# Performance work log

Hardware: AMD Instinct MI355X
Metric: run time of the kernel (lower is better)

Reference implementation:

```python
import jax, jax.numpy as jnp
import numpy as np

BATCH, SEQ, DIM = 32, 1024, 512

def setup_inputs() -> dict:
    key = jax.random.key(0)
    k1, k2, k3 = jax.random.split(key, 3)
    scale = 1.0 / np.sqrt(DIM)
    return {
        "embedded_sequence": jax.random.normal(k1, (BATCH, SEQ, DIM), dtype=jnp.float32),
        "W_xh": jax.random.normal(k2, (DIM, DIM), dtype=jnp.float32) * scale,
        "W_hh": jax.random.normal(k3, (DIM, DIM), dtype=jnp.float32) * scale,
        "b": jnp.zeros((DIM,), dtype=jnp.float32),
    }

def reference(embedded_sequence, W_xh, W_hh, b):
    # SimpleRNN: h_t = tanh(x_t @ W_xh + h_{t-1} @ W_hh + b)
    B, T, D = embedded_sequence.shape
    # Precompute input projection for all timesteps (one big GEMM)
    xw = jnp.einsum('btd,de->bte', embedded_sequence, W_xh) + b  # [B,T,D]
    h0 = jnp.zeros((B, D), dtype=embedded_sequence.dtype)

    def step(h, xw_t):
        h_new = jnp.tanh(xw_t + h @ W_hh)
        return h_new, h_new

    h_final, seq_out = jax.lax.scan(step, h0, jnp.swapaxes(xw, 0, 1))  # scan over T
    seq_out = jnp.swapaxes(seq_out, 0, 1)  # [B,T,D]
    return (seq_out, h_final)
```

## Files before the change

### kernel.cpp

```cpp
#include <hip/hip_runtime.h>
#include <hip/hip_fp16.h>

#define BATCH 32
#define SEQ   1024
#define DIM   512

typedef _Float16 f16x8 __attribute__((ext_vector_type(8)));
typedef float    f32x4 __attribute__((ext_vector_type(4)));
typedef unsigned int u32x4 __attribute__((ext_vector_type(4)));

union UU4 { uint4 s; u32x4 v; };

static __device__ __forceinline__ float tanh_fast(float x) {
    float e = __expf(2.0f * x);
    return 1.0f - 2.0f / (e + 1.0f);
}

__global__ void pack_w2(const float* __restrict__ W0, __half* __restrict__ Wp0,
                        const float* __restrict__ W1, __half* __restrict__ Wp1) {
    int blk = blockIdx.x;
    const float* W  = (blk < 512) ? W0 : W1;
    __half*      Wp = (blk < 512) ? Wp0 : Wp1;
    int id = (blk & 511) * blockDim.x + threadIdx.x;
    int n = id & 511;
    int k = id >> 9;
    Wp[((k >> 5) * 512 + n) * 32 + ((k >> 3) & 3) * 8 + (k & 7)] = __float2half(W[k * 512 + n]);
}

__global__ __launch_bounds__(1024, 1) void gemm_xw(const float* __restrict__ X,
                                                   const __half* __restrict__ Wp,
                                                   const float* __restrict__ bias,
                                                   float* __restrict__ out) {
    const int nb   = blockIdx.x;
    const int mb   = blockIdx.y;
    const int lane = threadIdx.x & 63;
    const int wave = threadIdx.x >> 6;
    const int q    = lane >> 4;
    const int r16  = lane & 15;
    const int row  = mb * 256 + wave * 16 + r16;

    const float4* Xf4  = (const float4*)X;
    const uint4*  WpU4 = (const uint4*)Wp;

    f32x4 acc[16];
    #pragma unroll
    for (int nt = 0; nt < 16; ++nt) acc[nt] = (f32x4){0.f, 0.f, 0.f, 0.f};

    #pragma unroll 2
    for (int kb = 0; kb < 16; ++kb) {
        float4 a0 = Xf4[row * 128 + kb * 8 + q * 2];
        float4 a1 = Xf4[row * 128 + kb * 8 + q * 2 + 1];
        f16x8 af;
        af[0] = (_Float16)a0.x; af[1] = (_Float16)a0.y;
        af[2] = (_Float16)a0.z; af[3] = (_Float16)a0.w;
        af[4] = (_Float16)a1.x; af[5] = (_Float16)a1.y;
        af[6] = (_Float16)a1.z; af[7] = (_Float16)a1.w;
        #pragma unroll
        for (int nt = 0; nt < 16; ++nt) {
            int col = nb * 256 + nt * 16 + r16;
            UU4 tmp; tmp.s = WpU4[(kb * 512 + col) * 4 + q];
            acc[nt] = __builtin_amdgcn_mfma_f32_16x16x32_f16(
                af, __builtin_bit_cast(f16x8, tmp.v), acc[nt], 0, 0, 0);
        }
    }

    const int rbase = mb * 256 + wave * 16 + q * 4;
    #pragma unroll
    for (int nt = 0; nt < 16; ++nt) {
        int col = nb * 256 + nt * 16 + r16;
        float bv = bias[col];
        #pragma unroll
        for (int rr = 0; rr < 4; ++rr) {
            out[(size_t)(rbase + rr) * 512 + col] = acc[nt][rr] + bv;
        }
    }
}

__global__ __launch_bounds__(512, 2) void rnn_rec(const uint4* __restrict__ Wp4,
                                                  float* __restrict__ out) {
    extern __shared__ char smem[];
    uint4*  LBS = (uint4*)smem;
    __half* hb  = (__half*)(smem + 131072);

    const int b    = blockIdx.x;
    const int t    = threadIdx.x;
    const int lane = t & 63;
    const int w    = t >> 6;
    const int q    = lane >> 4;
    const int r16  = lane & 15;

    #pragma unroll
    for (int j = 0; j < 16; ++j) {
        int kb  = 12 + (j >> 2);
        int col = w * 64 + (j & 3) * 16 + r16;
        LBS[j * 512 + t] = Wp4[(kb * 512 + col) * 4 + q];
    }

    u32x4 Bf[48];
    #pragma unroll
    for (int kb = 0; kb < 12; ++kb) {
        #pragma unroll
        for (int nt = 0; nt < 4; ++nt) {
            int col = w * 64 + nt * 16 + r16;
            UU4 tmp; tmp.s = Wp4[(kb * 512 + col) * 4 + q];
            Bf[kb * 4 + nt] = tmp.v;
        }
    }
    #pragma unroll
    for (int i = 0; i < 48; ++i) asm volatile("" : "+a"(Bf[i]));

    float* orow = out + (size_t)b * SEQ * DIM;
    const int c = w * 64 + q * 16 + r16;

    float xw = orow[c];
    float h  = tanh_fast(xw);
    orow[c] = h;
    hb[c] = __float2half(h);
    xw = orow[DIM + c];
    __syncthreads();

    #pragma unroll 1
    for (int step = 1; step < SEQ; ++step) {
        orow += DIM;
        const __half* ha = hb + (((step & 1) ^ 1) << 9);

        f32x4 m[4];
        #pragma unroll
        for (int i = 0; i < 4; ++i) m[i] = (f32x4){0.f, 0.f, 0.f, 0.f};

        #pragma unroll
        for (int s = 0; s < 4; ++s) {
            f16x8 af = *(const f16x8*)(ha + (12 + s) * 32 + q * 8);
            #pragma unroll
            for (int nt = 0; nt < 4; ++nt) {
                UU4 tmp; tmp.s = LBS[(s * 4 + nt) * 512 + t];
                m[nt] = __builtin_amdgcn_mfma_f32_16x16x32_f16(
                    af, __builtin_bit_cast(f16x8, tmp.v), m[nt], 0, 0, 0);
            }
        }
        #pragma unroll
        for (int kb = 0; kb < 12; ++kb) {
            f16x8 af = *(const f16x8*)(ha + kb * 32 + q * 8);
            #pragma unroll
            for (int nt = 0; nt < 4; ++nt) {
                m[nt] = __builtin_amdgcn_mfma_f32_16x16x32_f16(
                    af, __builtin_bit_cast(f16x8, Bf[kb * 4 + nt]), m[nt], 0, 0, 0);
            }
        }

        float v = (q == 0 ? m[0][0] : q == 1 ? m[1][0] : q == 2 ? m[2][0] : m[3][0]) + xw;
        h = tanh_fast(v);

        orow[c] = h;
        __half* hw = hb + ((step & 1) << 9);
        hw[c] = __float2half(h);
        xw = orow[DIM + c];
        __syncthreads();
    }

    float* hf = out + (size_t)BATCH * SEQ * DIM + (size_t)b * DIM;
    hf[c] = h;
}

extern "C" void kernel_launch(void* const* d_in, const int* in_sizes, int n_in,
                              void* d_out, int out_size, void* d_ws, size_t ws_size,
                              hipStream_t stream) {
    const float* X    = (const float*)d_in[0];
    const float* Wxh  = (const float*)d_in[1];
    const float* Whh  = (const float*)d_in[2];
    const float* bias = (const float*)d_in[3];
    float* out = (float*)d_out;

    __half* WpXh = (__half*)d_ws;
    __half* WpHh = (__half*)((char*)d_ws + (512u << 10));

    (void)hipFuncSetAttribute((const void*)rnn_rec,
                              hipFuncAttributeMaxDynamicSharedMemorySize, 133120);

    pack_w2<<<1024, 512, 0, stream>>>(Wxh, WpXh, Whh, WpHh);
    gemm_xw<<<dim3(2, 128), 1024, 0, stream>>>(X, WpXh, bias, out);
    rnn_rec<<<BATCH, 512, 133120, stream>>>((const uint4*)WpHh, out);
}
```

Baseline: 1.480 ms.

## Fuse input GEMM into recurrence kernel with per-chunk flag gating

Merges the input-projection GEMM and the recurrent scan into one launch. The first 32 blocks run the recurrence while the other 512 blocks compute 128-timestep chunks of xW+b and publish completion through atomic flags. Recurrence blocks spin-wait on a chunk's flag only when they reach it, so the GEMM overlaps the serial scan instead of running before it. This relies on the recurrence blocks being co-resident with the GEMM blocks and adds spin-waits and atomics. It also needs 133KB of shared memory for every block, including the GEMM blocks, which may limit how many GEMM blocks can be resident at once.

```diff
diff --git a/kernel.cpp b/kernel.cpp
--- a/kernel.cpp
+++ b/kernel.cpp
@@ -16,8 +16,19 @@
     return 1.0f - 2.0f / (e + 1.0f);
 }
 
+static __device__ __forceinline__ void gate_wait(unsigned int* flags, int idx) {
+    if (threadIdx.x == 0) {
+        while (__hip_atomic_load(&flags[idx], __ATOMIC_ACQUIRE,
+                                 __HIP_MEMORY_SCOPE_AGENT) < 2u)
+            __builtin_amdgcn_s_sleep(8);
+    }
+    __syncthreads();
+}
+
 __global__ void pack_w2(const float* __restrict__ W0, __half* __restrict__ Wp0,
-                        const float* __restrict__ W1, __half* __restrict__ Wp1) {
+                        const float* __restrict__ W1, __half* __restrict__ Wp1,
+                        unsigned int* __restrict__ flags) {
+    if (blockIdx.x == 0 && threadIdx.x < 256) flags[threadIdx.x] = 0u;
     int blk = blockIdx.x;
     const float* W  = (blk < 512) ? W0 : W1;
     __half*      Wp = (blk < 512) ? Wp0 : Wp1;
@@ -27,73 +38,81 @@
     Wp[((k >> 5) * 512 + n) * 32 + ((k >> 3) & 3) * 8 + (k & 7)] = __float2half(W[k * 512 + n]);
 }
 
-__global__ __launch_bounds__(1024, 1) void gemm_xw(const float* __restrict__ X,
-                                                   const __half* __restrict__ Wp,
-                                                   const float* __restrict__ bias,
-                                                   float* __restrict__ out) {
-    const int nb   = blockIdx.x;
-    const int mb   = blockIdx.y;
+__global__ __launch_bounds__(512, 2) void fused_rnn(
+        const float* __restrict__ X, const __half* __restrict__ WpXh,
+        const float* __restrict__ bias, const uint4* __restrict__ WpHh4,
+        float* __restrict__ out, unsigned int* __restrict__ flags)
+{
+    extern __shared__ char smem[];
     const int lane = threadIdx.x & 63;
-    const int wave = threadIdx.x >> 6;
+    const int w    = threadIdx.x >> 6;
     const int q    = lane >> 4;
     const int r16  = lane & 15;
-    const int row  = mb * 256 + wave * 16 + r16;
-
-    const float4* Xf4  = (const float4*)X;
-    const uint4*  WpU4 = (const uint4*)Wp;
-
-    f32x4 acc[16];
-    #pragma unroll
-    for (int nt = 0; nt < 16; ++nt) acc[nt] = (f32x4){0.f, 0.f, 0.f, 0.f};
-
-    #pragma unroll 2
-    for (int kb = 0; kb < 16; ++kb) {
-        float4 a0 = Xf4[row * 128 + kb * 8 + q * 2];
-        float4 a1 = Xf4[row * 128 + kb * 8 + q * 2 + 1];
-        f16x8 af;
-        af[0] = (_Float16)a0.x; af[1] = (_Float16)a0.y;
-        af[2] = (_Float16)a0.z; af[3] = (_Float16)a0.w;
-        af[4] = (_Float16)a1.x; af[5] = (_Float16)a1.y;
-        af[6] = (_Float16)a1.z; af[7] = (_Float16)a1.w;
+
+    if (blockIdx.x >= 32) {
+        const int g  = (int)blockIdx.x - 32;
+        const int nb = g & 1;
+        const int sg = g >> 1;
+        const int bg = sg & 31;
+        const int st = sg >> 5;
+        const int row = bg * 1024 + st * 128 + w * 16 + r16;
+
+        const float4* Xf4  = (const float4*)X;
+        const uint4*  WpU4 = (const uint4*)WpXh;
+
+        f32x4 acc[16];
+        #pragma unroll
+        for (int nt = 0; nt < 16; ++nt) acc[nt] = (f32x4){0.f, 0.f, 0.f, 0.f};
+
+        #pragma unroll 2
+        for (int kb = 0; kb < 16; ++kb) {
+            float4 a0 = Xf4[row * 128 + kb * 8 + q * 2];
+            float4 a1 = Xf4[row * 128 + kb * 8 + q * 2 + 1];
+            f16x8 af;
+            af[0] = (_Float16)a0.x; af[1] = (_Float16)a0.y;
+            af[2] = (_Float16)a0.z; af[3] = (_Float16)a0.w;
+            af[4] = (_Float16)a1.x; af[5] = (_Float16)a1.y;
+            af[6] = (_Float16)a1.z; af[7] = (_Float16)a1.w;
+            #pragma unroll
+            for (int nt = 0; nt < 16; ++nt) {
+                int col = nb * 256 + nt * 16 + r16;
+                UU4 tmp; tmp.s = WpU4[(kb * 512 + col) * 4 + q];
+                acc[nt] = __builtin_amdgcn_mfma_f32_16x16x32_f16(
+                    af, __builtin_bit_cast(f16x8, tmp.v), acc[nt], 0, 0, 0);
+            }
+        }
+
+        const int rbase = bg * 1024 + st * 128 + w * 16 + q * 4;
         #pragma unroll
         for (int nt = 0; nt < 16; ++nt) {
             int col = nb * 256 + nt * 16 + r16;
-            UU4 tmp; tmp.s = WpU4[(kb * 512 + col) * 4 + q];
-            acc[nt] = __builtin_amdgcn_mfma_f32_16x16x32_f16(
-                af, __builtin_bit_cast(f16x8, tmp.v), acc[nt], 0, 0, 0);
-        }
-    }
-
-    const int rbase = mb * 256 + wave * 16 + q * 4;
-    #pragma unroll
-    for (int nt = 0; nt < 16; ++nt) {
-        int col = nb * 256 + nt * 16 + r16;
-        float bv = bias[col];
-        #pragma unroll
-        for (int rr = 0; rr < 4; ++rr) {
-            out[(size_t)(rbase + rr) * 512 + col] = acc[nt][rr] + bv;
-        }
-    }
-}
-
-__global__ __launch_bounds__(512, 2) void rnn_rec(const uint4* __restrict__ Wp4,
-                                                  float* __restrict__ out) {
-    extern __shared__ char smem[];
+            float bv = bias[col];
+            #pragma unroll
+            for (int rr = 0; rr < 4; ++rr) {
+                out[(size_t)(rbase + rr) * 512 + col] = acc[nt][rr] + bv;
+            }
+        }
+
+        __syncthreads();
+        if (threadIdx.x == 0) {
+            __threadfence();
+            __hip_atomic_fetch_add(&flags[sg], 1u, __ATOMIC_RELEASE,
+                                   __HIP_MEMORY_SCOPE_AGENT);
+        }
+        return;
+    }
+
     uint4*  LBS = (uint4*)smem;
     __half* hb  = (__half*)(smem + 131072);
 
-    const int b    = blockIdx.x;
-    const int t    = threadIdx.x;
-    const int lane = t & 63;
-    const int w    = t >> 6;
-    const int q    = lane >> 4;
-    const int r16  = lane & 15;
+    const int b = blockIdx.x;
+    const int t = threadIdx.x;
 
     #pragma unroll
     for (int j = 0; j < 16; ++j) {
         int kb  = 12 + (j >> 2);
         int col = w * 64 + (j & 3) * 16 + r16;
-        LBS[j * 512 + t] = Wp4[(kb * 512 + col) * 4 + q];
+        LBS[j * 512 + t] = WpHh4[(kb * 512 + col) * 4 + q];
     }
 
     u32x4 Bf[48];
@@ -102,7 +121,7 @@
         #pragma unroll
         for (int nt = 0; nt < 4; ++nt) {
             int col = w * 64 + nt * 16 + r16;
-            UU4 tmp; tmp.s = Wp4[(kb * 512 + col) * 4 + q];
+            UU4 tmp; tmp.s = WpHh4[(kb * 512 + col) * 4 + q];
             Bf[kb * 4 + nt] = tmp.v;
         }
     }
@@ -111,6 +130,8 @@
 
     float* orow = out + (size_t)b * SEQ * DIM;
     const int c = w * 64 + q * 16 + r16;
+
+    gate_wait(flags, 0 * 32 + b);
 
     float xw = orow[c];
     float h  = tanh_fast(xw);
@@ -154,6 +175,11 @@
         orow[c] = h;
         __half* hw = hb + ((step & 1) << 9);
         hw[c] = __float2half(h);
+
+        const int nstep = step + 1;
+        if ((nstep & 127) == 0 && nstep < SEQ)
+            gate_wait(flags, (nstep >> 7) * 32 + b);
+
         xw = orow[DIM + c];
         __syncthreads();
     }
@@ -173,11 +199,12 @@
 
     __half* WpXh = (__half*)d_ws;
     __half* WpHh = (__half*)((char*)d_ws + (512u << 10));
-
-    (void)hipFuncSetAttribute((const void*)rnn_rec,
+    unsigned int* flags = (unsigned int*)((char*)d_ws + (1024u << 10));
+
+    (void)hipFuncSetAttribute((const void*)fused_rnn,
                               hipFuncAttributeMaxDynamicSharedMemorySize, 133120);
 
-    pack_w2<<<1024, 512, 0, stream>>>(Wxh, WpXh, Whh, WpHh);
-    gemm_xw<<<dim3(2, 128), 1024, 0, stream>>>(X, WpXh, bias, out);
-    rnn_rec<<<BATCH, 512, 133120, stream>>>((const uint4*)WpHh, out);
-}
+    pack_w2<<<1024, 512, 0, stream>>>(Wxh, WpXh, Whh, WpHh, flags);
+    fused_rnn<<<544, 512, 133120, stream>>>(X, WpXh, bias,
+                                            (const uint4*)WpHh, out, flags);
+}
```

Measured after the change: 1.439 ms. 2.8% less time.
